# Optimization experiments

Hardware: AMD Instinct MI355X
Metric: run time of the kernel (lower is better)

The kernel has to match this reference:

```python
import jax, jax.numpy as jnp
import numpy as np

B, N, D = 65536, 2, 512


def _ln(x, g, b, eps=1e-5):
    mu = jnp.mean(x, axis=-1, keepdims=True)
    var = jnp.mean((x - mu) ** 2, axis=-1, keepdims=True)
    return (x - mu) * jax.lax.rsqrt(var + eps) * g + b


def setup_inputs() -> dict:
    key = jax.random.key(0)
    ks = jax.random.split(key, 20)
    s = 0.02
    p = {
        'x': jax.random.normal(ks[0], (B, N, D), jnp.float32),
        'wq': jax.random.normal(ks[1], (D, D), jnp.float32) * s,
        'bq': jnp.zeros((D,), jnp.float32),
        'wk': jax.random.normal(ks[2], (D, D), jnp.float32) * s,
        'bk': jnp.zeros((D,), jnp.float32),
        'wv': jax.random.normal(ks[3], (D, D), jnp.float32) * s,
        'bv': jnp.zeros((D,), jnp.float32),
        'wo': jax.random.normal(ks[4], (D, D), jnp.float32) * s,
        'bo': jnp.zeros((D,), jnp.float32),
        'g1': jnp.ones((D,), jnp.float32),
        'be1': jnp.zeros((D,), jnp.float32),
        'wf1': jax.random.normal(ks[5], (D, 2 * D), jnp.float32) * s,
        'bf1': jnp.zeros((2 * D,), jnp.float32),
        'wf2': jax.random.normal(ks[6], (2 * D, D), jnp.float32) * s,
        'bf2': jnp.zeros((D,), jnp.float32),
        'g2': jnp.ones((D,), jnp.float32),
        'be2': jnp.zeros((D,), jnp.float32),
        'ws1': jax.random.normal(ks[7], (D, D), jnp.float32) * s,
        'bs1': jnp.zeros((D,), jnp.float32),
        'ws2': jax.random.normal(ks[8], (D, 1), jnp.float32) * s,
        'bs2': jnp.zeros((1,), jnp.float32),
    }
    return p


def reference(x, wq, bq, wk, bk, wv, bv, wo, bo, g1, be1, wf1, bf1, wf2, bf2, g2, be2, ws1, bs1, ws2, bs2):
    # Q/K/V projections: (B, N, D)
    q = x @ wq + bq
    k = x @ wk + bk
    v = x @ wv + bv
    scale = jnp.sqrt(jnp.float32(D)) + 1e-8
    # attention scores over tiny N x N (N=2)
    attn = jnp.einsum('bnd,bmd->bnm', q, k) / scale
    attn = jax.nn.leaky_relu(attn, negative_slope=0.2)
    attn = jax.nn.softmax(attn, axis=-1)
    out = jnp.einsum('bnm,bmd->bnd', attn, v) @ wo + bo
    # residual + norm1 (dropout = identity in eval)
    h = _ln(x + out, g1, be1)
    # FFN
    ffn = jax.nn.relu(h @ wf1 + bf1) @ wf2 + bf2
    refined = _ln(h + ffn, g2, be2)
    # score MLP -> attention pooling
    scores = (jax.nn.relu(refined @ ws1 + bs1) @ ws2 + bs2)[..., 0]  # (B, N)
    alpha = jax.nn.softmax(scores, axis=-1)
    fused = jnp.einsum('bn,bnd->bd', alpha, refined)
    # final parameter-free layer_norm
    mu = jnp.mean(fused, axis=-1, keepdims=True)
    var = jnp.mean((fused - mu) ** 2, axis=-1, keepdims=True)
    fused = (fused - mu) * jax.lax.rsqrt(var + 1e-5)
    return (fused, alpha, refined)
```

## Files before the change

kernel.cpp:

```cpp
#include <hip/hip_runtime.h>


typedef __attribute__((ext_vector_type(8))) short s8v;
typedef __attribute__((ext_vector_type(4))) float f4v;

#define MFMA16 __builtin_amdgcn_mfma_f32_16x16x32_bf16

__device__ __forceinline__ unsigned short f2bf(float f) {
  union { float f; unsigned u; } v; v.f = f;
  unsigned u = v.u;
  unsigned r = (u + 0x7FFFu + ((u >> 16) & 1u)) >> 16;
  return (unsigned short)r;
}
__device__ __forceinline__ float bf2f(unsigned short h) {
  union { unsigned u; float f; } v; v.u = ((unsigned)h) << 16;
  return v.f;
}

__device__ __forceinline__ void gload_lds16(const void* g, void* l) {
  __builtin_amdgcn_global_load_lds(
      (const __attribute__((address_space(1))) unsigned int*)g,
      (__attribute__((address_space(3))) unsigned int*)l, 16, 0, 0);
}

#define STAGE64_F32(SRC) do { \
    const float4* sp_ = (const float4*)(SRC); \
    _Pragma("unroll") \
    for (int p_ = 0; p_ < 16; ++p_) { \
      int idx_ = p_ * 512 + tid; \
      int r_ = idx_ >> 7, c_ = (idx_ & 127) << 2; \
      float4 v_ = sp_[idx_]; \
      uint2 w_; \
      w_.x = (unsigned)f2bf(v_.x) | ((unsigned)f2bf(v_.y) << 16); \
      w_.y = (unsigned)f2bf(v_.z) | ((unsigned)f2bf(v_.w) << 16); \
      *(uint2*)(xs + r_ * 520 + c_) = w_; \
    } } while (0)

#define KLOOP_512(BT, LDB) do { \
    const int ar0_ = (rw * 32 + l15) * 520, ar1_ = (rw * 32 + 16 + l15) * 520; \
    for (int ks_ = 0; ks_ < 16; ++ks_) { \
      int k0_ = ks_ * 32 + quad * 8; \
      s8v a0_ = *(const s8v*)(xs + ar0_ + k0_); \
      s8v a1_ = *(const s8v*)(xs + ar1_ + k0_); \
      _Pragma("unroll") \
      for (int ct_ = 0; ct_ < 8; ++ct_) { \
        int n_ = cw * 128 + ct_ * 16 + l15; \
        s8v b_ = *(const s8v*)((BT) + n_ * (LDB) + k0_); \
        acc[0][ct_] = MFMA16(a0_, b_, acc[0][ct_], 0, 0, 0); \
        acc[1][ct_] = MFMA16(a1_, b_, acc[1][ct_], 0, 0, 0); \
      } \
    } } while (0)


__global__ void tr32(const float* __restrict__ in, float* __restrict__ out) {
  int idx = blockIdx.x * 256 + threadIdx.x;
  int d = idx >> 9, j = idx & 511;
  out[idx] = in[j * 512 + d];
}

__global__ void nt_small(const float* __restrict__ A, const float* __restrict__ B,
                         unsigned short* __restrict__ C) {
  __shared__ float As[64][68], Bs[64][68];
  int tx = threadIdx.x & 15, ty = threadIdx.x >> 4;
  int i0 = blockIdx.x * 64, j0 = blockIdx.y * 64;
  float acc[4][4] = {};
  for (int d0 = 0; d0 < 512; d0 += 64) {
    #pragma unroll
    for (int p = 0; p < 4; ++p) {
      int idx = p * 256 + threadIdx.x;
      int r = idx >> 4, c = (idx & 15) << 2;
      *(float4*)&As[r][c] = *(const float4*)&A[(i0 + r) * 512 + d0 + c];
      *(float4*)&Bs[r][c] = *(const float4*)&B[(j0 + r) * 512 + d0 + c];
    }
    __syncthreads();
    for (int dd = 0; dd < 64; ++dd) {
      float ar[4], br[4];
      #pragma unroll
      for (int r = 0; r < 4; ++r) ar[r] = As[ty * 4 + r][dd];
      #pragma unroll
      for (int c = 0; c < 4; ++c) br[c] = Bs[tx * 4 + c][dd];
      #pragma unroll
      for (int r = 0; r < 4; ++r)
        #pragma unroll
        for (int c = 0; c < 4; ++c) acc[r][c] += ar[r] * br[c];
    }
    __syncthreads();
  }
  #pragma unroll
  for (int r = 0; r < 4; ++r)
    #pragma unroll
    for (int c = 0; c < 4; ++c)
      C[(i0 + ty * 4 + r) * 512 + j0 + tx * 4 + c] = f2bf(acc[r][c]);
}

__global__ void trcvt(const float* __restrict__ in, unsigned short* __restrict__ out,
                      int K, int N) {
  int idx = blockIdx.x * 256 + threadIdx.x;
  if (idx >= K * N) return;
  int n = idx / K, k = idx - n * K;
  out[idx] = f2bf(in[(size_t)k * N + n]);
}

__global__ void vecprep(const float* __restrict__ wq, const float* __restrict__ wk,
                        const float* __restrict__ wo, const float* __restrict__ bq,
                        const float* __restrict__ bk, const float* __restrict__ bv,
                        float* __restrict__ uvec, float* __restrict__ wvec,
                        float* __restrict__ cvec, float* __restrict__ bvo) {
  int t = threadIdx.x;
  if (blockIdx.x == 0) {
    float s = 0.f; for (int d = 0; d < 512; ++d) s += wq[t * 512 + d] * bk[d];
    uvec[t] = s;
  } else if (blockIdx.x == 1) {
    float s = 0.f; for (int d = 0; d < 512; ++d) s += wk[t * 512 + d] * bq[d];
    wvec[t] = s;
  } else if (blockIdx.x == 2) {
    float s = 0.f; for (int j = 0; j < 512; ++j) s += bv[j] * wo[j * 512 + t];
    bvo[t] = s;
  } else {
    __shared__ float red[512];
    red[t] = bq[t] * bk[t];
    __syncthreads();
    for (int o = 256; o; o >>= 1) { if (t < o) red[t] += red[t + o]; __syncthreads(); }
    if (t == 0) cvec[0] = red[0];
  }
}

__global__ __launch_bounds__(512, 2) void k1_attn(
    const float* __restrict__ x, const unsigned short* __restrict__ gqk,
    const float* __restrict__ uvec, const float* __restrict__ wvec,
    const float* __restrict__ cvec, float* __restrict__ attn) {
  __shared__ unsigned short xs[64 * 520];
  __shared__ float sbuf[32][2][2];
  __shared__ float rru[64];
  __shared__ float rrw[64];
  const int tid = threadIdx.x;
  const int wave = tid >> 6, lane = tid & 63, quad = lane >> 4, l15 = lane & 15;
  const int rw = wave >> 2, cw = wave & 3;
  const size_t row0 = (size_t)blockIdx.x * 64;

  if (tid < 128) ((float*)sbuf)[tid] = 0.f;
  else if (tid < 192) rru[tid - 128] = 0.f;
  else if (tid < 256) rrw[tid - 192] = 0.f;

  STAGE64_F32(x + row0 * 512);
  __syncthreads();

  {
    int row = tid >> 3, cb = (tid & 7) * 64;
    float su = 0.f, sw = 0.f;
    for (int c2 = 0; c2 < 64; ++c2) {
      float xv = bf2f(xs[row * 520 + cb + c2]);
      su += xv * uvec[cb + c2];
      sw += xv * wvec[cb + c2];
    }
    atomicAdd(&rru[row], su);
    atomicAdd(&rrw[row], sw);
  }

  f4v acc[2][8] = {};
  KLOOP_512(gqk, 512);

  float part[2][4][2] = {};
  #pragma unroll
  for (int t = 0; t < 2; ++t) {
    #pragma unroll
    for (int ct = 0; ct < 8; ++ct) {
      int col = cw * 128 + ct * 16 + l15;
      #pragma unroll
      for (int g = 0; g < 4; ++g) {
        int m = rw * 32 + t * 16 + quad * 4 + g;
        float zv = acc[t][ct][g];
        int b2 = m & ~1;
        part[t][g][0] += bf2f(xs[b2 * 520 + col]) * zv;
        part[t][g][1] += bf2f(xs[(b2 + 1) * 520 + col]) * zv;
      }
    }
  }
  #pragma unroll
  for (int t = 0; t < 2; ++t)
    #pragma unroll
    for (int g = 0; g < 4; ++g) {
      int m = rw * 32 + t * 16 + quad * 4 + g;
      atomicAdd(&sbuf[m >> 1][0][m & 1], part[t][g][0]);
      atomicAdd(&sbuf[m >> 1][1][m & 1], part[t][g][1]);
    }
  __syncthreads();

  if (tid < 64) {
    int bl = tid >> 1, nn = tid & 1;
    float cc = cvec[0];
    float ru = rru[bl * 2 + nn];
    float scale = sqrtf(512.f) + 1e-8f;
    float s0 = (sbuf[bl][nn][0] + ru + rrw[bl * 2 + 0] + cc) / scale;
    float s1 = (sbuf[bl][nn][1] + ru + rrw[bl * 2 + 1] + cc) / scale;
    s0 = s0 > 0.f ? s0 : 0.2f * s0;
    s1 = s1 > 0.f ? s1 : 0.2f * s1;
    float mx = fmaxf(s0, s1);
    float e0 = expf(s0 - mx), e1 = expf(s1 - mx);
    float inv = 1.f / (e0 + e1);
    size_t gb = (size_t)blockIdx.x * 32 + bl;
    attn[gb * 4 + nn * 2 + 0] = e0 * inv;
    attn[gb * 4 + nn * 2 + 1] = e1 * inv;
  }
}

__global__ __launch_bounds__(512, 2) void k2_proj(
    const float* __restrict__ x, const unsigned short* __restrict__ wvoT,
    const float* __restrict__ bvo, const float* __restrict__ bo,
    const float* __restrict__ attn, const float* __restrict__ g1,
    const float* __restrict__ be1, unsigned short* __restrict__ hout) {
  __shared__ unsigned short xs[64 * 520];
  __shared__ unsigned short vos[64 * 520];
  const int tid = threadIdx.x;
  const int wave = tid >> 6, lane = tid & 63, quad = lane >> 4, l15 = lane & 15;
  const int rw = wave >> 2, cw = wave & 3;
  const size_t row0 = (size_t)blockIdx.x * 64;

  STAGE64_F32(x + row0 * 512);
  __syncthreads();

  f4v acc[2][8] = {};
  KLOOP_512(wvoT, 512);

  #pragma unroll
  for (int t = 0; t < 2; ++t)
    #pragma unroll
    for (int ct = 0; ct < 8; ++ct) {
      int col = cw * 128 + ct * 16 + l15;
      float bb = bvo[col];
      #pragma unroll
      for (int g = 0; g < 4; ++g) {
        int m = rw * 32 + t * 16 + quad * 4 + g;
        vos[m * 520 + col] = f2bf(acc[t][ct][g] + bb);
      }
    }
  __syncthreads();

  for (int rr = 0; rr < 8; ++rr) {
    int r = wave * 8 + rr;
    size_t grow = row0 + r;
    size_t gb = (size_t)blockIdx.x * 32 + (r >> 1);
    float a0 = attn[gb * 4 + (r & 1) * 2 + 0];
    float a1 = attn[gb * 4 + (r & 1) * 2 + 1];
    int c0 = lane * 8;
    int b2 = r & ~1;
    float v[8]; float s = 0.f, s2 = 0.f;
    #pragma unroll
    for (int j = 0; j < 8; ++j) {
      int c = c0 + j;
      float val = bf2f(xs[r * 520 + c]) + a0 * bf2f(vos[b2 * 520 + c]) +
                  a1 * bf2f(vos[(b2 + 1) * 520 + c]) + bo[c];
      v[j] = val; s += val; s2 += val * val;
    }
    #pragma unroll
    for (int o = 32; o; o >>= 1) { s += __shfl_xor(s, o); s2 += __shfl_xor(s2, o); }
    float mu = s * (1.f / 512.f);
    float var = s2 * (1.f / 512.f) - mu * mu;
    float rs = rsqrtf(var + 1e-5f);
    unsigned short o8[8];
    #pragma unroll
    for (int j = 0; j < 8; ++j)
      o8[j] = f2bf((v[j] - mu) * rs * g1[c0 + j] + be1[c0 + j]);
    int4 w4;
    w4.x = (int)((unsigned)o8[0] | ((unsigned)o8[1] << 16));
    w4.y = (int)((unsigned)o8[2] | ((unsigned)o8[3] << 16));
    w4.z = (int)((unsigned)o8[4] | ((unsigned)o8[5] << 16));
    w4.w = (int)((unsigned)o8[6] | ((unsigned)o8[7] << 16));
    *(int4*)(hout + grow * 512 + c0) = w4;
  }
}

__global__ __launch_bounds__(512, 4) void k3a_ffn1(
    const unsigned short* __restrict__ h, const unsigned short* __restrict__ wf1T,
    const float* __restrict__ bf1, unsigned short* __restrict__ hid) {
  __shared__ unsigned short As[64 * 64];
  __shared__ unsigned short Bs[512 * 64];
  const int tid = threadIdx.x;
  const int wave = tid >> 6, lane = tid & 63, quad = lane >> 4, l15 = lane & 15;
  const int rw = wave >> 2, cw = wave & 3;
  const size_t row0 = (size_t)blockIdx.x * 64;
  const int n0 = blockIdx.y * 512;

  const int ar = tid >> 3;
  const int ao = (tid & 7) ^ (ar & 7);
  const char* asrc = (const char*)(h + (row0 + ar) * 512) + ao * 16;
  char* adst = (char*)As + (size_t)wave * 1024;

  const int aswz = (l15 & 7);
  const int abase0 = (rw * 32 + l15) * 128;
  const int abase1 = (rw * 32 + 16 + l15) * 128;
  const int bbase = (cw * 128 + l15) * 128;

  f4v acc[2][8] = {};
  for (int ks = 0; ks < 8; ++ks) {
    const int k0 = ks * 64;
    gload_lds16(asrc + k0 * 2, adst);
    #pragma unroll
    for (int it = 0; it < 8; ++it) {
      int c = it * 512 + tid;
      int bn = c >> 3;
      int bo = (c & 7) ^ (bn & 7);
      const char* bsrc = (const char*)(wf1T + (size_t)(n0 + bn) * 512 + k0) + bo * 16;
      gload_lds16(bsrc, (char*)Bs + it * 8192 + wave * 1024);
    }
    __syncthreads();
    #pragma unroll
    for (int kk = 0; kk < 2; ++kk) {
      const int d = kk * 4 + quad;
      const int so = ((d ^ aswz) << 4);
      s8v a0 = *(const s8v*)((const char*)As + abase0 + so);
      s8v a1 = *(const s8v*)((const char*)As + abase1 + so);
      #pragma unroll
      for (int ct = 0; ct < 8; ++ct) {
        s8v b = *(const s8v*)((const char*)Bs + bbase + ct * 2048 + so);
        acc[0][ct] = MFMA16(a0, b, acc[0][ct], 0, 0, 0);
        acc[1][ct] = MFMA16(a1, b, acc[1][ct], 0, 0, 0);
      }
    }
    __syncthreads();
  }

  #pragma unroll
  for (int ct = 0; ct < 8; ++ct) {
    int col = n0 + cw * 128 + ct * 16 + l15;
    float bb = bf1[col];
    #pragma unroll
    for (int t = 0; t < 2; ++t)
      #pragma unroll
      for (int g = 0; g < 4; ++g) {
        size_t row = row0 + rw * 32 + t * 16 + quad * 4 + g;
        hid[row * 1024 + col] = f2bf(fmaxf(acc[t][ct][g] + bb, 0.f));
      }
  }
}

__global__ __launch_bounds__(512, 4) void k3b_ffn2(
    const unsigned short* hid, const unsigned short* __restrict__ wf2T,
    const float* __restrict__ bf2, const unsigned short* __restrict__ h,
    const float* __restrict__ g2, const float* __restrict__ be2,
    float* refined) {
  __shared__ unsigned short As[64 * 64];
  __shared__ unsigned short Bs[512 * 64];
  __shared__ float rsum[64], rsq[64];
  const int tid = threadIdx.x;
  const int wave = tid >> 6, lane = tid & 63, quad = lane >> 4, l15 = lane & 15;
  const int rw = wave >> 2, cw = wave & 3;
  const size_t row0 = (size_t)blockIdx.x * 64;

  if (tid < 64) { rsum[tid] = 0.f; rsq[tid] = 0.f; }

  const int ar = tid >> 3;
  const int ao = (tid & 7) ^ (ar & 7);
  const char* asrc = (const char*)(hid + (row0 + ar) * 1024) + ao * 16;
  char* adst = (char*)As + (size_t)wave * 1024;

  const int aswz = (l15 & 7);
  const int abase0 = (rw * 32 + l15) * 128;
  const int abase1 = (rw * 32 + 16 + l15) * 128;
  const int bbase = (cw * 128 + l15) * 128;

  f4v acc[2][8] = {};
  for (int ks = 0; ks < 16; ++ks) {
    const int k0 = ks * 64;
    gload_lds16(asrc + k0 * 2, adst);
    #pragma unroll
    for (int it = 0; it < 8; ++it) {
      int c = it * 512 + tid;
      int bn = c >> 3;
      int bo = (c & 7) ^ (bn & 7);
      const char* bsrc = (const char*)(wf2T + (size_t)bn * 1024 + k0) + bo * 16;
      gload_lds16(bsrc, (char*)Bs + it * 8192 + wave * 1024);
    }
    __syncthreads();
    #pragma unroll
    for (int kk = 0; kk < 2; ++kk) {
      const int d = kk * 4 + quad;
      const int so = ((d ^ aswz) << 4);
      s8v a0 = *(const s8v*)((const char*)As + abase0 + so);
      s8v a1 = *(const s8v*)((const char*)As + abase1 + so);
      #pragma unroll
      for (int ct = 0; ct < 8; ++ct) {
        s8v b = *(const s8v*)((const char*)Bs + bbase + ct * 2048 + so);
        acc[0][ct] = MFMA16(a0, b, acc[0][ct], 0, 0, 0);
        acc[1][ct] = MFMA16(a1, b, acc[1][ct], 0, 0, 0);
      }
    }
    __syncthreads();
  }

  #pragma unroll
  for (int t = 0; t < 2; ++t)
    #pragma unroll
    for (int g = 0; g < 4; ++g) {
      int lrow = rw * 32 + t * 16 + quad * 4 + g;
      size_t row = row0 + lrow;
      float ps = 0.f, ps2 = 0.f;
      #pragma unroll
      for (int ct = 0; ct < 8; ++ct) {
        int col = cw * 128 + ct * 16 + l15;
        float v = acc[t][ct][g] + bf2[col] + bf2f(h[row * 512 + col]);
        acc[t][ct][g] = v;
        ps += v; ps2 += v * v;
      }
      #pragma unroll
      for (int o = 1; o < 16; o <<= 1) {
        ps += __shfl_xor(ps, o);
        ps2 += __shfl_xor(ps2, o);
      }
      if (l15 == 0) { atomicAdd(&rsum[lrow], ps); atomicAdd(&rsq[lrow], ps2); }
    }
  __syncthreads();

  #pragma unroll
  for (int t = 0; t < 2; ++t)
    #pragma unroll
    for (int g = 0; g < 4; ++g) {
      int lrow = rw * 32 + t * 16 + quad * 4 + g;
      size_t row = row0 + lrow;
      float mu = rsum[lrow] * (1.f / 512.f);
      float var = rsq[lrow] * (1.f / 512.f) - mu * mu;
      float rs = rsqrtf(var + 1e-5f);
      #pragma unroll
      for (int ct = 0; ct < 8; ++ct) {
        int col = cw * 128 + ct * 16 + l15;
        refined[row * 512 + col] = (acc[t][ct][g] - mu) * rs * g2[col] + be2[col];
      }
    }
}

__global__ __launch_bounds__(512, 2) void k4_pool(
    const float* __restrict__ refined, const unsigned short* __restrict__ ws1T,
    const float* __restrict__ bs1, const float* __restrict__ ws2,
    const float* __restrict__ bs2, float* __restrict__ fused,
    float* __restrict__ alpha) {
  __shared__ unsigned short xs[64 * 520];
  __shared__ float sc[64];
  __shared__ float al[2][32];
  const int tid = threadIdx.x;
  const int wave = tid >> 6, lane = tid & 63, quad = lane >> 4, l15 = lane & 15;
  const int rw = wave >> 2, cw = wave & 3;
  const size_t row0 = (size_t)blockIdx.x * 64;

  if (tid < 64) sc[tid] = 0.f;
  STAGE64_F32(refined + row0 * 512);
  __syncthreads();

  f4v acc[2][8] = {};
  KLOOP_512(ws1T, 512);

  float ps[2][4] = {};
  #pragma unroll
  for (int t = 0; t < 2; ++t)
    #pragma unroll
    for (int ct = 0; ct < 8; ++ct) {
      int col = cw * 128 + ct * 16 + l15;
      float b1 = bs1[col], w2 = ws2[col];
      #pragma unroll
      for (int g = 0; g < 4; ++g) {
        float v = fmaxf(acc[t][ct][g] + b1, 0.f);
        ps[t][g] += v * w2;
      }
    }
  #pragma unroll
  for (int t = 0; t < 2; ++t)
    #pragma unroll
    for (int g = 0; g < 4; ++g) {
      int m = rw * 32 + t * 16 + quad * 4 + g;
      atomicAdd(&sc[m], ps[t][g]);
    }
  __syncthreads();

  if (tid < 32) {
    float s0 = sc[tid * 2 + 0] + bs2[0];
    float s1 = sc[tid * 2 + 1] + bs2[0];
    float mx = fmaxf(s0, s1);
    float e0 = expf(s0 - mx), e1 = expf(s1 - mx);
    float inv = 1.f / (e0 + e1);
    float a0 = e0 * inv, a1 = e1 * inv;
    al[0][tid] = a0; al[1][tid] = a1;
    size_t gb = (size_t)blockIdx.x * 32 + tid;
    alpha[gb * 2 + 0] = a0;
    alpha[gb * 2 + 1] = a1;
  }
  __syncthreads();

  for (int rr = 0; rr < 4; ++rr) {
    int fb = wave * 4 + rr;
    float a0 = al[0][fb], a1 = al[1][fb];
    int c0 = lane * 8;
    float v[8]; float s = 0.f, s2 = 0.f;
    #pragma unroll
    for (int j = 0; j < 8; ++j) {
      int c = c0 + j;
      float val = a0 * bf2f(xs[(fb * 2) * 520 + c]) + a1 * bf2f(xs[(fb * 2 + 1) * 520 + c]);
      v[j] = val; s += val; s2 += val * val;
    }
    #pragma unroll
    for (int o = 32; o; o >>= 1) { s += __shfl_xor(s, o); s2 += __shfl_xor(s2, o); }
    float mu = s * (1.f / 512.f);
    float var = s2 * (1.f / 512.f) - mu * mu;
    float rs = rsqrtf(var + 1e-5f);
    size_t gb = (size_t)blockIdx.x * 32 + fb;
    float4 f0, f1;
    f0.x = (v[0] - mu) * rs; f0.y = (v[1] - mu) * rs;
    f0.z = (v[2] - mu) * rs; f0.w = (v[3] - mu) * rs;
    f1.x = (v[4] - mu) * rs; f1.y = (v[5] - mu) * rs;
    f1.z = (v[6] - mu) * rs; f1.w = (v[7] - mu) * rs;
    *(float4*)(fused + gb * 512 + c0) = f0;
    *(float4*)(fused + gb * 512 + c0 + 4) = f1;
  }
}

extern "C" void kernel_launch(void* const* d_in, const int* in_sizes, int n_in,
                              void* d_out, int out_size, void* d_ws, size_t ws_size,
                              hipStream_t stream) {
  const float* x   = (const float*)d_in[0];
  const float* wq  = (const float*)d_in[1];
  const float* bq  = (const float*)d_in[2];
  const float* wk  = (const float*)d_in[3];
  const float* bk  = (const float*)d_in[4];
  const float* wv  = (const float*)d_in[5];
  const float* bv  = (const float*)d_in[6];
  const float* wo  = (const float*)d_in[7];
  const float* bo  = (const float*)d_in[8];
  const float* g1  = (const float*)d_in[9];
  const float* be1 = (const float*)d_in[10];
  const float* wf1 = (const float*)d_in[11];
  const float* bf1 = (const float*)d_in[12];
  const float* wf2 = (const float*)d_in[13];
  const float* bf2 = (const float*)d_in[14];
  const float* g2  = (const float*)d_in[15];
  const float* be2 = (const float*)d_in[16];
  const float* ws1 = (const float*)d_in[17];
  const float* bs1 = (const float*)d_in[18];
  const float* ws2 = (const float*)d_in[19];
  const float* bs2 = (const float*)d_in[20];

  char* ws = (char*)d_ws;
  float*          attn = (float*)(ws);
  unsigned short* gqk  = (unsigned short*)(ws + (1u << 20));
  unsigned short* wvoT = (unsigned short*)(ws + (1u << 20) + 524288);
  float*          woT  = (float*)(ws + (2u << 20));
  unsigned short* wf1T = (unsigned short*)(ws + (3u << 20));
  unsigned short* wf2T = (unsigned short*)(ws + (4u << 20));
  unsigned short* ws1T = (unsigned short*)(ws + (5u << 20));
  float*          uvec = (float*)(ws + (5u << 20) + 524288);
  float*          wvec = uvec + 1024;
  float*          cvec = wvec + 1024;
  float*          bvo  = cvec + 1024;
  unsigned short* h    = (unsigned short*)(ws + (16u << 20));

  float* fused_out   = (float*)d_out;
  float* alpha_out   = fused_out + (size_t)65536 * 512;
  float* refined_out = alpha_out + (size_t)65536 * 2;
  unsigned short* hid = (unsigned short*)refined_out;

  tr32<<<dim3(1024), dim3(256), 0, stream>>>(wo, woT);
  nt_small<<<dim3(8, 8), dim3(256), 0, stream>>>(wq, wk, gqk);
  nt_small<<<dim3(8, 8), dim3(256), 0, stream>>>(woT, wv, wvoT);
  trcvt<<<dim3(2048), dim3(256), 0, stream>>>(wf1, wf1T, 512, 1024);
  trcvt<<<dim3(2048), dim3(256), 0, stream>>>(wf2, wf2T, 1024, 512);
  trcvt<<<dim3(1024), dim3(256), 0, stream>>>(ws1, ws1T, 512, 512);
  vecprep<<<dim3(4), dim3(512), 0, stream>>>(wq, wk, wo, bq, bk, bv, uvec, wvec, cvec, bvo);

  k1_attn<<<dim3(2048), dim3(512), 0, stream>>>(x, gqk, uvec, wvec, cvec, attn);
  k2_proj<<<dim3(2048), dim3(512), 0, stream>>>(x, wvoT, bvo, bo, attn, g1, be1, h);
  k3a_ffn1<<<dim3(2048, 2), dim3(512), 0, stream>>>(h, wf1T, bf1, hid);
  k3b_ffn2<<<dim3(2048), dim3(512), 0, stream>>>(hid, wf2T, bf2, h, g2, be2, refined_out);
  k4_pool<<<dim3(2048), dim3(512), 0, stream>>>(refined_out, ws1T, bs1, ws2, bs2,
                                                fused_out, alpha_out);
}
```

Measured before the change: 2.208 ms.

## Stage B-operand weight tiles into LDS with double-buffered async loads

The k1, k2 and k4 GEMM loops used to read their weight operand straight from global memory for every MFMA. They now copy 32-wide K chunks of the weights into a swizzled, double-buffered LDS area using global_load_lds and prefetch the next chunk while the current one is computed. This is meant to hide global load latency and cut redundant global traffic. The cost is a barrier every K step and more LDS per block: 64KB extra in k1 and k4, while k2 reuses its vos buffer. That extra LDS may prevent two blocks from fitting per CU in k1 and k4.

New measurement: 1.842 ms. 1.2x faster.

```diff
diff --git a/kernel.cpp b/kernel.cpp
--- a/kernel.cpp
+++ b/kernel.cpp
@@ -36,20 +36,32 @@
       *(uint2*)(xs + r_ * 520 + c_) = w_; \
     } } while (0)
 
-#define KLOOP_512(BT, LDB) do { \
+#define BSTAGE_CHUNK(BT, K0, DST) do { \
+    _Pragma("unroll") \
+    for (int it_ = 0; it_ < 4; ++it_) \
+      gload_lds16((const char*)((BT) + (size_t)(it_ * 128 + brow) * 512 + (K0)) + boff, \
+                  (DST) + (it_ * 512 + tid) * 16); \
+  } while (0)
+
+#define KLOOP_STAGED(BT) do { \
     const int ar0_ = (rw * 32 + l15) * 520, ar1_ = (rw * 32 + 16 + l15) * 520; \
+    const int bsw_ = ((quad ^ (l15 & 3) ^ ((l15 >> 2) & 3)) << 4); \
+    const int bro_ = (cw * 128 + l15) * 64; \
     for (int ks_ = 0; ks_ < 16; ++ks_) { \
-      int k0_ = ks_ * 32 + quad * 8; \
-      s8v a0_ = *(const s8v*)(xs + ar0_ + k0_); \
-      s8v a1_ = *(const s8v*)(xs + ar1_ + k0_); \
+      char* cur_ = bsl + (ks_ & 1) * 32768; \
+      if (ks_ < 15) BSTAGE_CHUNK(BT, (ks_ + 1) * 32, bsl + ((ks_ & 1) ^ 1) * 32768); \
+      int ka_ = ks_ * 32 + quad * 8; \
+      s8v a0_ = *(const s8v*)(xs + ar0_ + ka_); \
+      s8v a1_ = *(const s8v*)(xs + ar1_ + ka_); \
       _Pragma("unroll") \
       for (int ct_ = 0; ct_ < 8; ++ct_) { \
-        int n_ = cw * 128 + ct_ * 16 + l15; \
-        s8v b_ = *(const s8v*)((BT) + n_ * (LDB) + k0_); \
+        s8v b_ = *(const s8v*)(cur_ + bro_ + ct_ * 1024 + bsw_); \
         acc[0][ct_] = MFMA16(a0_, b_, acc[0][ct_], 0, 0, 0); \
         acc[1][ct_] = MFMA16(a1_, b_, acc[1][ct_], 0, 0, 0); \
       } \
-    } } while (0)
+      __syncthreads(); \
+    } \
+  } while (0)
 
 
 __global__ void tr32(const float* __restrict__ in, float* __restrict__ out) {
@@ -129,7 +141,8 @@
     const float* __restrict__ x, const unsigned short* __restrict__ gqk,
     const float* __restrict__ uvec, const float* __restrict__ wvec,
     const float* __restrict__ cvec, float* __restrict__ attn) {
-  __shared__ unsigned short xs[64 * 520];
+  __shared__ __align__(16) unsigned short xs[64 * 520];
+  __shared__ __align__(16) char bsb[65536];
   __shared__ float sbuf[32][2][2];
   __shared__ float rru[64];
   __shared__ float rrw[64];
@@ -137,11 +150,15 @@
   const int wave = tid >> 6, lane = tid & 63, quad = lane >> 4, l15 = lane & 15;
   const int rw = wave >> 2, cw = wave & 3;
   const size_t row0 = (size_t)blockIdx.x * 64;
+  char* bsl = bsb;
+  const int brow = tid >> 2;
+  const int boff = (((tid & 3) ^ (brow & 3) ^ ((brow >> 2) & 3)) << 4);
 
   if (tid < 128) ((float*)sbuf)[tid] = 0.f;
   else if (tid < 192) rru[tid - 128] = 0.f;
   else if (tid < 256) rrw[tid - 192] = 0.f;
 
+  BSTAGE_CHUNK(gqk, 0, bsl);
   STAGE64_F32(x + row0 * 512);
   __syncthreads();
 
@@ -158,7 +175,7 @@
   }
 
   f4v acc[2][8] = {};
-  KLOOP_512(gqk, 512);
+  KLOOP_STAGED(gqk);
 
   float part[2][4][2] = {};
   #pragma unroll
@@ -209,18 +226,23 @@
     const float* __restrict__ bvo, const float* __restrict__ bo,
     const float* __restrict__ attn, const float* __restrict__ g1,
     const float* __restrict__ be1, unsigned short* __restrict__ hout) {
-  __shared__ unsigned short xs[64 * 520];
-  __shared__ unsigned short vos[64 * 520];
+  __shared__ __align__(16) unsigned short xs[64 * 520];
+  __shared__ __align__(16) unsigned short bss[64 * 520];
   const int tid = threadIdx.x;
   const int wave = tid >> 6, lane = tid & 63, quad = lane >> 4, l15 = lane & 15;
   const int rw = wave >> 2, cw = wave & 3;
   const size_t row0 = (size_t)blockIdx.x * 64;
-
+  char* bsl = (char*)bss;
+  unsigned short* vos = bss;
+  const int brow = tid >> 2;
+  const int boff = (((tid & 3) ^ (brow & 3) ^ ((brow >> 2) & 3)) << 4);
+
+  BSTAGE_CHUNK(wvoT, 0, bsl);
   STAGE64_F32(x + row0 * 512);
   __syncthreads();
 
   f4v acc[2][8] = {};
-  KLOOP_512(wvoT, 512);
+  KLOOP_STAGED(wvoT);
 
   #pragma unroll
   for (int t = 0; t < 2; ++t)
@@ -273,8 +295,8 @@
 __global__ __launch_bounds__(512, 4) void k3a_ffn1(
     const unsigned short* __restrict__ h, const unsigned short* __restrict__ wf1T,
     const float* __restrict__ bf1, unsigned short* __restrict__ hid) {
-  __shared__ unsigned short As[64 * 64];
-  __shared__ unsigned short Bs[512 * 64];
+  __shared__ __align__(16) unsigned short As[64 * 64];
+  __shared__ __align__(16) unsigned short Bs[512 * 64];
   const int tid = threadIdx.x;
   const int wave = tid >> 6, lane = tid & 63, quad = lane >> 4, l15 = lane & 15;
   const int rw = wave >> 2, cw = wave & 3;
@@ -339,8 +361,8 @@
     const float* __restrict__ bf2, const unsigned short* __restrict__ h,
     const float* __restrict__ g2, const float* __restrict__ be2,
     float* refined) {
-  __shared__ unsigned short As[64 * 64];
-  __shared__ unsigned short Bs[512 * 64];
+  __shared__ __align__(16) unsigned short As[64 * 64];
+  __shared__ __align__(16) unsigned short Bs[512 * 64];
   __shared__ float rsum[64], rsq[64];
   const int tid = threadIdx.x;
   const int wave = tid >> 6, lane = tid & 63, quad = lane >> 4, l15 = lane & 15;
@@ -433,20 +455,25 @@
     const float* __restrict__ bs1, const float* __restrict__ ws2,
     const float* __restrict__ bs2, float* __restrict__ fused,
     float* __restrict__ alpha) {
-  __shared__ unsigned short xs[64 * 520];
+  __shared__ __align__(16) unsigned short xs[64 * 520];
+  __shared__ __align__(16) char bsb[65536];
   __shared__ float sc[64];
   __shared__ float al[2][32];
   const int tid = threadIdx.x;
   const int wave = tid >> 6, lane = tid & 63, quad = lane >> 4, l15 = lane & 15;
   const int rw = wave >> 2, cw = wave & 3;
   const size_t row0 = (size_t)blockIdx.x * 64;
+  char* bsl = bsb;
+  const int brow = tid >> 2;
+  const int boff = (((tid & 3) ^ (brow & 3) ^ ((brow >> 2) & 3)) << 4);
 
   if (tid < 64) sc[tid] = 0.f;
+  BSTAGE_CHUNK(ws1T, 0, bsl);
   STAGE64_F32(refined + row0 * 512);
   __syncthreads();
 
   f4v acc[2][8] = {};
-  KLOOP_512(ws1T, 512);
+  KLOOP_STAGED(ws1T);
 
   float ps[2][4] = {};
   #pragma unroll
```

## Unify GEMMs on swizzled LDS-staged pipeline with pre-converted bf16 inputs

Applied to the files above, without the earlier changes.

Adds a pass that converts x to bf16 once into the fused output buffer, then rewrites k1, k2 and k4 to use the same k3-style chunked GEMM. That GEMM stages swizzled A and B tiles into LDS with global_load_lds, in place of reading weights straight from global and staging the full row in padded LDS. k2's epilogue now works on accumulators in registers with shuffle-reduced LayerNorm stats and stages output through LDS for coalesced stores. k3b also writes a bf16 copy of refined so k4 reads half the bytes. The smaller LDS footprint allows 4 blocks per CU, at the cost of an extra conversion pass and more per-chunk syncs.

New measurement: 1.837 ms. 1.2x faster.

```diff
diff --git a/kernel.cpp b/kernel.cpp
--- a/kernel.cpp
+++ b/kernel.cpp
@@ -23,34 +23,73 @@
       (__attribute__((address_space(3))) unsigned int*)l, 16, 0, 0);
 }
 
-#define STAGE64_F32(SRC) do { \
-    const float4* sp_ = (const float4*)(SRC); \
+#define GEMM_CHUNKS(BBASE, LDB_ELT, NCHUNK) \
+  for (int ks_ = 0; ks_ < (NCHUNK); ++ks_) { \
+    const int k0_ = ks_ * 64; \
+    gload_lds16(asrc + (size_t)k0_ * 2, adst); \
     _Pragma("unroll") \
-    for (int p_ = 0; p_ < 16; ++p_) { \
-      int idx_ = p_ * 512 + tid; \
-      int r_ = idx_ >> 7, c_ = (idx_ & 127) << 2; \
-      float4 v_ = sp_[idx_]; \
-      uint2 w_; \
-      w_.x = (unsigned)f2bf(v_.x) | ((unsigned)f2bf(v_.y) << 16); \
-      w_.y = (unsigned)f2bf(v_.z) | ((unsigned)f2bf(v_.w) << 16); \
-      *(uint2*)(xs + r_ * 520 + c_) = w_; \
-    } } while (0)
-
-#define KLOOP_512(BT, LDB) do { \
-    const int ar0_ = (rw * 32 + l15) * 520, ar1_ = (rw * 32 + 16 + l15) * 520; \
-    for (int ks_ = 0; ks_ < 16; ++ks_) { \
-      int k0_ = ks_ * 32 + quad * 8; \
-      s8v a0_ = *(const s8v*)(xs + ar0_ + k0_); \
-      s8v a1_ = *(const s8v*)(xs + ar1_ + k0_); \
+    for (int it_ = 0; it_ < 8; ++it_) { \
+      int c_ = it_ * 512 + tid; \
+      int bn_ = c_ >> 3; \
+      int bo_ = (c_ & 7) ^ (bn_ & 7); \
+      gload_lds16((const char*)((BBASE) + (size_t)bn_ * (LDB_ELT) + k0_) + bo_ * 16, \
+                  (char*)Bs + it_ * 8192 + wave * 1024); \
+    } \
+    __syncthreads(); \
+    _Pragma("unroll") \
+    for (int kk_ = 0; kk_ < 2; ++kk_) { \
+      const int d_ = kk_ * 4 + quad; \
+      const int so_ = ((d_ ^ aswz) << 4); \
+      s8v a0_ = *(const s8v*)((const char*)As + abase0 + so_); \
+      s8v a1_ = *(const s8v*)((const char*)As + abase1 + so_); \
       _Pragma("unroll") \
       for (int ct_ = 0; ct_ < 8; ++ct_) { \
-        int n_ = cw * 128 + ct_ * 16 + l15; \
-        s8v b_ = *(const s8v*)((BT) + n_ * (LDB) + k0_); \
+        s8v b_ = *(const s8v*)((const char*)Bs + bbase + ct_ * 2048 + so_); \
         acc[0][ct_] = MFMA16(a0_, b_, acc[0][ct_], 0, 0, 0); \
         acc[1][ct_] = MFMA16(a1_, b_, acc[1][ct_], 0, 0, 0); \
       } \
+    } \
+    __syncthreads(); \
+  }
+
+#define GEMM_LOCALS(ASRC_BF, LDA_ELT) \
+  const int ar_ = tid >> 3; \
+  const int ao_ = (tid & 7) ^ (ar_ & 7); \
+  const char* asrc = (const char*)((ASRC_BF) + (size_t)(row0 + ar_) * (LDA_ELT)) + ao_ * 16; \
+  char* adst = (char*)As + (size_t)wave * 1024; \
+  const int aswz = (l15 & 7); \
+  const int abase0 = (rw * 32 + l15) * 128; \
+  const int abase1 = (rw * 32 + 16 + l15) * 128; \
+  const int bbase = (cw * 128 + l15) * 128;
+
+#define STAGE_XT(SRCBF) do { \
+    _Pragma("unroll") \
+    for (int it_ = 0; it_ < 8; ++it_) { \
+      int c_ = it_ * 512 + tid; \
+      int r_ = c_ >> 6, s_ = c_ & 63; \
+      int sp_ = s_ ^ (r_ & 7); \
+      gload_lds16((const char*)((SRCBF) + (size_t)(row0 + r_) * 512) + sp_ * 16, \
+                  (char*)Bs + it_ * 8192 + wave * 1024); \
     } } while (0)
 
+#define XT_AT(r, col) \
+  bf2f(Bs[(r) * 512 + ((((col) >> 3) ^ ((r) & 7)) << 3) + ((col) & 7)])
+
+
+__global__ __launch_bounds__(256) void cvt_bf(const float* __restrict__ x,
+                                              unsigned short* __restrict__ xbf) {
+  int idx = blockIdx.x * 256 + threadIdx.x;
+  const float4* xp = (const float4*)x;
+  uint2* op = (uint2*)xbf;
+  #pragma unroll
+  for (int p = 0; p < 32; ++p) {
+    float4 v = xp[(size_t)p * 524288 + idx];
+    uint2 w;
+    w.x = (unsigned)f2bf(v.x) | ((unsigned)f2bf(v.y) << 16);
+    w.y = (unsigned)f2bf(v.z) | ((unsigned)f2bf(v.w) << 16);
+    op[(size_t)p * 524288 + idx] = w;
+  }
+}
 
 __global__ void tr32(const float* __restrict__ in, float* __restrict__ out) {
   int idx = blockIdx.x * 256 + threadIdx.x;
@@ -125,11 +164,12 @@
   }
 }
 
-__global__ __launch_bounds__(512, 2) void k1_attn(
-    const float* __restrict__ x, const unsigned short* __restrict__ gqk,
+__global__ __launch_bounds__(512, 4) void k1_attn(
+    const unsigned short* __restrict__ xbf, const unsigned short* __restrict__ gqk,
     const float* __restrict__ uvec, const float* __restrict__ wvec,
     const float* __restrict__ cvec, float* __restrict__ attn) {
-  __shared__ unsigned short xs[64 * 520];
+  __shared__ __align__(16) unsigned short As[64 * 64];
+  __shared__ __align__(16) unsigned short Bs[512 * 64];
   __shared__ float sbuf[32][2][2];
   __shared__ float rru[64];
   __shared__ float rrw[64];
@@ -142,14 +182,18 @@
   else if (tid < 192) rru[tid - 128] = 0.f;
   else if (tid < 256) rrw[tid - 192] = 0.f;
 
-  STAGE64_F32(x + row0 * 512);
+  GEMM_LOCALS(xbf, 512);
+  f4v acc[2][8] = {};
+  GEMM_CHUNKS(gqk, 512, 8);
+
+  STAGE_XT(xbf);
   __syncthreads();
 
   {
     int row = tid >> 3, cb = (tid & 7) * 64;
     float su = 0.f, sw = 0.f;
     for (int c2 = 0; c2 < 64; ++c2) {
-      float xv = bf2f(xs[row * 520 + cb + c2]);
+      float xv = XT_AT(row, cb + c2);
       su += xv * uvec[cb + c2];
       sw += xv * wvec[cb + c2];
     }
@@ -157,33 +201,41 @@
     atomicAdd(&rrw[row], sw);
   }
 
-  f4v acc[2][8] = {};
-  KLOOP_512(gqk, 512);
-
-  float part[2][4][2] = {};
-  #pragma unroll
-  for (int t = 0; t < 2; ++t) {
+  float part[2][2][2][2] = {};
+  #pragma unroll
+  for (int t = 0; t < 2; ++t)
     #pragma unroll
     for (int ct = 0; ct < 8; ++ct) {
       int col = cw * 128 + ct * 16 + l15;
       #pragma unroll
-      for (int g = 0; g < 4; ++g) {
-        int m = rw * 32 + t * 16 + quad * 4 + g;
-        float zv = acc[t][ct][g];
-        int b2 = m & ~1;
-        part[t][g][0] += bf2f(xs[b2 * 520 + col]) * zv;
-        part[t][g][1] += bf2f(xs[(b2 + 1) * 520 + col]) * zv;
-      }
-    }
-  }
-  #pragma unroll
-  for (int t = 0; t < 2; ++t)
-    #pragma unroll
-    for (int g = 0; g < 4; ++g) {
-      int m = rw * 32 + t * 16 + quad * 4 + g;
-      atomicAdd(&sbuf[m >> 1][0][m & 1], part[t][g][0]);
-      atomicAdd(&sbuf[m >> 1][1][m & 1], part[t][g][1]);
-    }
+      for (int p = 0; p < 2; ++p) {
+        int b2 = rw * 32 + t * 16 + quad * 4 + 2 * p;
+        float x0 = XT_AT(b2, col);
+        float x1 = XT_AT(b2 + 1, col);
+        float z0 = acc[t][ct][2 * p + 0];
+        float z1 = acc[t][ct][2 * p + 1];
+        part[t][p][0][0] += x0 * z0;
+        part[t][p][0][1] += x0 * z1;
+        part[t][p][1][0] += x1 * z0;
+        part[t][p][1][1] += x1 * z1;
+      }
+    }
+  #pragma unroll
+  for (int t = 0; t < 2; ++t)
+    #pragma unroll
+    for (int p = 0; p < 2; ++p)
+      #pragma unroll
+      for (int n = 0; n < 2; ++n)
+        #pragma unroll
+        for (int m = 0; m < 2; ++m) {
+          float v = part[t][p][n][m];
+          v += __shfl_xor(v, 1); v += __shfl_xor(v, 2);
+          v += __shfl_xor(v, 4); v += __shfl_xor(v, 8);
+          if (l15 == 0) {
+            int b = (rw * 32 + t * 16 + quad * 4 + 2 * p) >> 1;
+            atomicAdd(&sbuf[b][n][m], v);
+          }
+        }
   __syncthreads();
 
   if (tid < 64) {
@@ -204,121 +256,109 @@
   }
 }
 
-__global__ __launch_bounds__(512, 2) void k2_proj(
-    const float* __restrict__ x, const unsigned short* __restrict__ wvoT,
+__global__ __launch_bounds__(512, 4) void k2_proj(
+    const unsigned short* __restrict__ xbf, const unsigned short* __restrict__ wvoT,
     const float* __restrict__ bvo, const float* __restrict__ bo,
     const float* __restrict__ attn, const float* __restrict__ g1,
     const float* __restrict__ be1, unsigned short* __restrict__ hout) {
-  __shared__ unsigned short xs[64 * 520];
-  __shared__ unsigned short vos[64 * 520];
+  __shared__ __align__(16) unsigned short As[64 * 64];
+  __shared__ __align__(16) unsigned short Bs[512 * 64];
+  __shared__ float rsum[64], rsq[64];
   const int tid = threadIdx.x;
   const int wave = tid >> 6, lane = tid & 63, quad = lane >> 4, l15 = lane & 15;
   const int rw = wave >> 2, cw = wave & 3;
   const size_t row0 = (size_t)blockIdx.x * 64;
 
-  STAGE64_F32(x + row0 * 512);
-  __syncthreads();
-
+  if (tid < 64) { rsum[tid] = 0.f; rsq[tid] = 0.f; }
+
+  GEMM_LOCALS(xbf, 512);
   f4v acc[2][8] = {};
-  KLOOP_512(wvoT, 512);
-
-  #pragma unroll
-  for (int t = 0; t < 2; ++t)
-    #pragma unroll
-    for (int ct = 0; ct < 8; ++ct) {
-      int col = cw * 128 + ct * 16 + l15;
-      float bb = bvo[col];
-      #pragma unroll
-      for (int g = 0; g < 4; ++g) {
-        int m = rw * 32 + t * 16 + quad * 4 + g;
-        vos[m * 520 + col] = f2bf(acc[t][ct][g] + bb);
-      }
-    }
-  __syncthreads();
-
-  for (int rr = 0; rr < 8; ++rr) {
-    int r = wave * 8 + rr;
-    size_t grow = row0 + r;
-    size_t gb = (size_t)blockIdx.x * 32 + (r >> 1);
-    float a0 = attn[gb * 4 + (r & 1) * 2 + 0];
-    float a1 = attn[gb * 4 + (r & 1) * 2 + 1];
-    int c0 = lane * 8;
-    int b2 = r & ~1;
-    float v[8]; float s = 0.f, s2 = 0.f;
-    #pragma unroll
-    for (int j = 0; j < 8; ++j) {
-      int c = c0 + j;
-      float val = bf2f(xs[r * 520 + c]) + a0 * bf2f(vos[b2 * 520 + c]) +
-                  a1 * bf2f(vos[(b2 + 1) * 520 + c]) + bo[c];
-      v[j] = val; s += val; s2 += val * val;
-    }
-    #pragma unroll
-    for (int o = 32; o; o >>= 1) { s += __shfl_xor(s, o); s2 += __shfl_xor(s2, o); }
-    float mu = s * (1.f / 512.f);
-    float var = s2 * (1.f / 512.f) - mu * mu;
-    float rs = rsqrtf(var + 1e-5f);
-    unsigned short o8[8];
-    #pragma unroll
-    for (int j = 0; j < 8; ++j)
-      o8[j] = f2bf((v[j] - mu) * rs * g1[c0 + j] + be1[c0 + j]);
-    int4 w4;
-    w4.x = (int)((unsigned)o8[0] | ((unsigned)o8[1] << 16));
-    w4.y = (int)((unsigned)o8[2] | ((unsigned)o8[3] << 16));
-    w4.z = (int)((unsigned)o8[4] | ((unsigned)o8[5] << 16));
-    w4.w = (int)((unsigned)o8[6] | ((unsigned)o8[7] << 16));
-    *(int4*)(hout + grow * 512 + c0) = w4;
+  GEMM_CHUNKS(wvoT, 512, 8);
+
+  STAGE_XT(xbf);
+  __syncthreads();
+
+  float ps[2][4] = {}, ps2[2][4] = {};
+  #pragma unroll
+  for (int t = 0; t < 2; ++t)
+    #pragma unroll
+    for (int p = 0; p < 2; ++p) {
+      int b2 = rw * 32 + t * 16 + quad * 4 + 2 * p;
+      size_t gb = (size_t)blockIdx.x * 32 + (b2 >> 1);
+      float a00 = attn[gb * 4 + 0], a01 = attn[gb * 4 + 1];
+      float a10 = attn[gb * 4 + 2], a11 = attn[gb * 4 + 3];
+      #pragma unroll
+      for (int ct = 0; ct < 8; ++ct) {
+        int col = cw * 128 + ct * 16 + l15;
+        float bvoc = bvo[col], boc = bo[col];
+        float voA = acc[t][ct][2 * p + 0] + bvoc;
+        float voB = acc[t][ct][2 * p + 1] + bvoc;
+        float v0 = a00 * voA + a01 * voB + XT_AT(b2, col) + boc;
+        float v1 = a10 * voA + a11 * voB + XT_AT(b2 + 1, col) + boc;
+        acc[t][ct][2 * p + 0] = v0;
+        acc[t][ct][2 * p + 1] = v1;
+        ps[t][2 * p + 0] += v0; ps2[t][2 * p + 0] += v0 * v0;
+        ps[t][2 * p + 1] += v1; ps2[t][2 * p + 1] += v1 * v1;
+      }
+    }
+  #pragma unroll
+  for (int t = 0; t < 2; ++t)
+    #pragma unroll
+    for (int g = 0; g < 4; ++g) {
+      float s = ps[t][g], s2 = ps2[t][g];
+      s += __shfl_xor(s, 1); s += __shfl_xor(s, 2);
+      s += __shfl_xor(s, 4); s += __shfl_xor(s, 8);
+      s2 += __shfl_xor(s2, 1); s2 += __shfl_xor(s2, 2);
+      s2 += __shfl_xor(s2, 4); s2 += __shfl_xor(s2, 8);
+      if (l15 == 0) {
+        int lrow = rw * 32 + t * 16 + quad * 4 + g;
+        atomicAdd(&rsum[lrow], s);
+        atomicAdd(&rsq[lrow], s2);
+      }
+    }
+  __syncthreads();
+
+  #pragma unroll
+  for (int t = 0; t < 2; ++t)
+    #pragma unroll
+    for (int g = 0; g < 4; ++g) {
+      int lrow = rw * 32 + t * 16 + quad * 4 + g;
+      float mu = rsum[lrow] * (1.f / 512.f);
+      float var = rsq[lrow] * (1.f / 512.f) - mu * mu;
+      float rs = rsqrtf(var + 1e-5f);
+      #pragma unroll
+      for (int ct = 0; ct < 8; ++ct) {
+        int col = cw * 128 + ct * 16 + l15;
+        float hv = (acc[t][ct][g] - mu) * rs * g1[col] + be1[col];
+        Bs[lrow * 512 + (((col >> 3) ^ (lrow & 7)) << 3) + (col & 7)] = f2bf(hv);
+      }
+    }
+  __syncthreads();
+
+  #pragma unroll
+  for (int it = 0; it < 8; ++it) {
+    int c = it * 512 + tid;
+    int r = c >> 6, s = c & 63;
+    int sp = s ^ (r & 7);
+    *(int4*)(hout + (row0 + r) * 512 + s * 8) = *(const int4*)(Bs + r * 512 + sp * 8);
   }
 }
 
 __global__ __launch_bounds__(512, 4) void k3a_ffn1(
     const unsigned short* __restrict__ h, const unsigned short* __restrict__ wf1T,
     const float* __restrict__ bf1, unsigned short* __restrict__ hid) {
-  __shared__ unsigned short As[64 * 64];
-  __shared__ unsigned short Bs[512 * 64];
+  __shared__ __align__(16) unsigned short As[64 * 64];
+  __shared__ __align__(16) unsigned short Bs[512 * 64];
   const int tid = threadIdx.x;
   const int wave = tid >> 6, lane = tid & 63, quad = lane >> 4, l15 = lane & 15;
   const int rw = wave >> 2, cw = wave & 3;
   const size_t row0 = (size_t)blockIdx.x * 64;
   const int n0 = blockIdx.y * 512;
 
-  const int ar = tid >> 3;
-  const int ao = (tid & 7) ^ (ar & 7);
-  const char* asrc = (const char*)(h + (row0 + ar) * 512) + ao * 16;
-  char* adst = (char*)As + (size_t)wave * 1024;
-
-  const int aswz = (l15 & 7);
-  const int abase0 = (rw * 32 + l15) * 128;
-  const int abase1 = (rw * 32 + 16 + l15) * 128;
-  const int bbase = (cw * 128 + l15) * 128;
-
+  GEMM_LOCALS(h, 512);
+  const unsigned short* wb = wf1T + (size_t)n0 * 512;
   f4v acc[2][8] = {};
-  for (int ks = 0; ks < 8; ++ks) {
-    const int k0 = ks * 64;
-    gload_lds16(asrc + k0 * 2, adst);
-    #pragma unroll
-    for (int it = 0; it < 8; ++it) {
-      int c = it * 512 + tid;
-      int bn = c >> 3;
-      int bo = (c & 7) ^ (bn & 7);
-      const char* bsrc = (const char*)(wf1T + (size_t)(n0 + bn) * 512 + k0) + bo * 16;
-      gload_lds16(bsrc, (char*)Bs + it * 8192 + wave * 1024);
-    }
-    __syncthreads();
-    #pragma unroll
-    for (int kk = 0; kk < 2; ++kk) {
-      const int d = kk * 4 + quad;
-      const int so = ((d ^ aswz) << 4);
-      s8v a0 = *(const s8v*)((const char*)As + abase0 + so);
-      s8v a1 = *(const s8v*)((const char*)As + abase1 + so);
-      #pragma unroll
-      for (int ct = 0; ct < 8; ++ct) {
-        s8v b = *(const s8v*)((const char*)Bs + bbase + ct * 2048 + so);
-        acc[0][ct] = MFMA16(a0, b, acc[0][ct], 0, 0, 0);
-        acc[1][ct] = MFMA16(a1, b, acc[1][ct], 0, 0, 0);
-      }
-    }
-    __syncthreads();
-  }
+  GEMM_CHUNKS(wb, 512, 8);
 
   #pragma unroll
   for (int ct = 0; ct < 8; ++ct) {
@@ -336,11 +376,11 @@
 
 __global__ __launch_bounds__(512, 4) void k3b_ffn2(
     const unsigned short* hid, const unsigned short* __restrict__ wf2T,
-    const float* __restrict__ bf2, const unsigned short* __restrict__ h,
+    const float* __restrict__ bf2, unsigned short* h,
     const float* __restrict__ g2, const float* __restrict__ be2,
     float* refined) {
-  __shared__ unsigned short As[64 * 64];
-  __shared__ unsigned short Bs[512 * 64];
+  __shared__ __align__(16) unsigned short As[64 * 64];
+  __shared__ __align__(16) unsigned short Bs[512 * 64];
   __shared__ float rsum[64], rsq[64];
   const int tid = threadIdx.x;
   const int wave = tid >> 6, lane = tid & 63, quad = lane >> 4, l15 = lane & 15;
@@ -349,44 +389,9 @@
 
   if (tid < 64) { rsum[tid] = 0.f; rsq[tid] = 0.f; }
 
-  const int ar = tid >> 3;
-  const int ao = (tid & 7) ^ (ar & 7);
-  const char* asrc = (const char*)(hid + (row0 + ar) * 1024) + ao * 16;
-  char* adst = (char*)As + (size_t)wave * 1024;
-
-  const int aswz = (l15 & 7);
-  const int abase0 = (rw * 32 + l15) * 128;
-  const int abase1 = (rw * 32 + 16 + l15) * 128;
-  const int bbase = (cw * 128 + l15) * 128;
-
+  GEMM_LOCALS(hid, 1024);
   f4v acc[2][8] = {};
-  for (int ks = 0; ks < 16; ++ks) {
-    const int k0 = ks * 64;
-    gload_lds16(asrc + k0 * 2, adst);
-    #pragma unroll
-    for (int it = 0; it < 8; ++it) {
-      int c = it * 512 + tid;
-      int bn = c >> 3;
-      int bo = (c & 7) ^ (bn & 7);
-      const char* bsrc = (const char*)(wf2T + (size_t)bn * 1024 + k0) + bo * 16;
-      gload_lds16(bsrc, (char*)Bs + it * 8192 + wave * 1024);
-    }
-    __syncthreads();
-    #pragma unroll
-    for (int kk = 0; kk < 2; ++kk) {
-      const int d = kk * 4 + quad;
-      const int so = ((d ^ aswz) << 4);
-      s8v a0 = *(const s8v*)((const char*)As + abase0 + so);
-      s8v a1 = *(const s8v*)((const char*)As + abase1 + so);
-      #pragma unroll
-      for (int ct = 0; ct < 8; ++ct) {
-        s8v b = *(const s8v*)((const char*)Bs + bbase + ct * 2048 + so);
-        acc[0][ct] = MFMA16(a0, b, acc[0][ct], 0, 0, 0);
-        acc[1][ct] = MFMA16(a1, b, acc[1][ct], 0, 0, 0);
-      }
-    }
-    __syncthreads();
-  }
+  GEMM_CHUNKS(wf2T, 1024, 16);
 
   #pragma unroll
   for (int t = 0; t < 2; ++t)
@@ -423,17 +428,20 @@
       #pragma unroll
       for (int ct = 0; ct < 8; ++ct) {
         int col = cw * 128 + ct * 16 + l15;
-        refined[row * 512 + col] = (acc[t][ct][g] - mu) * rs * g2[col] + be2[col];
-      }
-    }
-}
-
-__global__ __launch_bounds__(512, 2) void k4_pool(
-    const float* __restrict__ refined, const unsigned short* __restrict__ ws1T,
+        float rv = (acc[t][ct][g] - mu) * rs * g2[col] + be2[col];
+        refined[row * 512 + col] = rv;
+        h[row * 512 + col] = f2bf(rv);
+      }
+    }
+}
+
+__global__ __launch_bounds__(512, 4) void k4_pool(
+    const unsigned short* __restrict__ refbf, const unsigned short* __restrict__ ws1T,
     const float* __restrict__ bs1, const float* __restrict__ ws2,
     const float* __restrict__ bs2, float* __restrict__ fused,
     float* __restrict__ alpha) {
-  __shared__ unsigned short xs[64 * 520];
+  __shared__ __align__(16) unsigned short As[64 * 64];
+  __shared__ __align__(16) unsigned short Bs[512 * 64];
   __shared__ float sc[64];
   __shared__ float al[2][32];
   const int tid = threadIdx.x;
@@ -442,11 +450,10 @@
   const size_t row0 = (size_t)blockIdx.x * 64;
 
   if (tid < 64) sc[tid] = 0.f;
-  STAGE64_F32(refined + row0 * 512);
-  __syncthreads();
-
+
+  GEMM_LOCALS(refbf, 512);
   f4v acc[2][8] = {};
-  KLOOP_512(ws1T, 512);
+  GEMM_CHUNKS(ws1T, 512, 8);
 
   float ps[2][4] = {};
   #pragma unroll
@@ -461,12 +468,20 @@
         ps[t][g] += v * w2;
       }
     }
+
+  STAGE_XT(refbf);
+
   #pragma unroll
   for (int t = 0; t < 2; ++t)
     #pragma unroll
     for (int g = 0; g < 4; ++g) {
-      int m = rw * 32 + t * 16 + quad * 4 + g;
-      atomicAdd(&sc[m], ps[t][g]);
+      float v = ps[t][g];
+      v += __shfl_xor(v, 1); v += __shfl_xor(v, 2);
+      v += __shfl_xor(v, 4); v += __shfl_xor(v, 8);
+      if (l15 == 0) {
+        int m = rw * 32 + t * 16 + quad * 4 + g;
+        atomicAdd(&sc[m], v);
+      }
     }
   __syncthreads();
 
@@ -487,12 +502,13 @@
   for (int rr = 0; rr < 4; ++rr) {
     int fb = wave * 4 + rr;
     float a0 = al[0][fb], a1 = al[1][fb];
-    int c0 = lane * 8;
+    int r0 = fb * 2, r1 = fb * 2 + 1;
+    s8v v0 = *(const s8v*)(Bs + r0 * 512 + ((lane ^ (r0 & 7)) << 3));
+    s8v v1 = *(const s8v*)(Bs + r1 * 512 + ((lane ^ (r1 & 7)) << 3));
     float v[8]; float s = 0.f, s2 = 0.f;
     #pragma unroll
     for (int j = 0; j < 8; ++j) {
-      int c = c0 + j;
-      float val = a0 * bf2f(xs[(fb * 2) * 520 + c]) + a1 * bf2f(xs[(fb * 2 + 1) * 520 + c]);
+      float val = a0 * bf2f((unsigned short)v0[j]) + a1 * bf2f((unsigned short)v1[j]);
       v[j] = val; s += val; s2 += val * val;
     }
     #pragma unroll
@@ -501,6 +517,7 @@
     float var = s2 * (1.f / 512.f) - mu * mu;
     float rs = rsqrtf(var + 1e-5f);
     size_t gb = (size_t)blockIdx.x * 32 + fb;
+    int c0 = lane * 8;
     float4 f0, f1;
     f0.x = (v[0] - mu) * rs; f0.y = (v[1] - mu) * rs;
     f0.z = (v[2] - mu) * rs; f0.w = (v[3] - mu) * rs;
@@ -554,6 +571,8 @@
   float* alpha_out   = fused_out + (size_t)65536 * 512;
   float* refined_out = alpha_out + (size_t)65536 * 2;
   unsigned short* hid = (unsigned short*)refined_out;
+  unsigned short* xbf = (unsigned short*)fused_out;
+  unsigned short* refbf = h;
 
   tr32<<<dim3(1024), dim3(256), 0, stream>>>(wo, woT);
   nt_small<<<dim3(8, 8), dim3(256), 0, stream>>>(wq, wk, gqk);
@@ -562,11 +581,12 @@
   trcvt<<<dim3(2048), dim3(256), 0, stream>>>(wf2, wf2T, 1024, 512);
   trcvt<<<dim3(1024), dim3(256), 0, stream>>>(ws1, ws1T, 512, 512);
   vecprep<<<dim3(4), dim3(512), 0, stream>>>(wq, wk, wo, bq, bk, bv, uvec, wvec, cvec, bvo);
-
-  k1_attn<<<dim3(2048), dim3(512), 0, stream>>>(x, gqk, uvec, wvec, cvec, attn);
-  k2_proj<<<dim3(2048), dim3(512), 0, stream>>>(x, wvoT, bvo, bo, attn, g1, be1, h);
+  cvt_bf<<<dim3(2048), dim3(256), 0, stream>>>(x, xbf);
+
+  k1_attn<<<dim3(2048), dim3(512), 0, stream>>>(xbf, gqk, uvec, wvec, cvec, attn);
+  k2_proj<<<dim3(2048), dim3(512), 0, stream>>>(xbf, wvoT, bvo, bo, attn, g1, be1, h);
   k3a_ffn1<<<dim3(2048, 2), dim3(512), 0, stream>>>(h, wf1T, bf1, hid);
   k3b_ffn2<<<dim3(2048), dim3(512), 0, stream>>>(hid, wf2T, bf2, h, g2, be2, refined_out);
-  k4_pool<<<dim3(2048), dim3(512), 0, stream>>>(refined_out, ws1T, bs1, ws2, bs2,
+  k4_pool<<<dim3(2048), dim3(512), 0, stream>>>(refbf, ws1T, bs1, ws2, bs2,
                                                 fused_out, alpha_out);
 }
```
